# Kernel tuning notes

Hardware: AMD Instinct MI355X
Metric: run time of the kernel (lower is better)

The kernel has to match this reference:

```python
import jax, jax.numpy as jnp
import numpy as np

N0, N1, N2, N3 = 65536, 16384, 4096, 1024
S = 9  # 3x3 kernel -> 9 selections (self + 8 directions)


def _edges(key, n):
    # each node has S incoming edges, one per selection
    src = jax.random.randint(key, (n * S,), 0, n)
    dst = jnp.repeat(jnp.arange(n), S)
    sel = jnp.tile(jnp.arange(S), n)
    return src, dst, sel


def setup_inputs() -> dict:
    key = jax.random.key(0)
    ks = jax.random.split(key, 40)
    inp = {}
    inp["x"] = jax.random.normal(ks[0], (N0, 3), jnp.float32)
    sizes = [N0, N1, N2, N3]
    for l, n in enumerate(sizes):
        src, dst, sel = _edges(ks[1 + l], n)
        inp[f"src{l}"] = src
        inp[f"dst{l}"] = dst
        inp[f"sel{l}"] = sel
        inp[f"interp{l}"] = jax.random.uniform(ks[5 + l], (n * S,), jnp.float32)
    inp["clus0"] = jnp.arange(N0) // 4
    inp["clus1"] = jnp.arange(N1) // 4
    inp["clus2"] = jnp.arange(N2) // 4
    dims = [(3, 3), (3, 64), (64, 64), (64, 128), (128, 128), (128, 256), (256, 256), (256, 256), (256, 256), (256, 512)]
    for i, (ci, co) in enumerate(dims):
        kw = ks[10 + 2 * i]
        kb = ks[11 + 2 * i]
        if i == 0:  # conv1 is kernel_size=1 -> single weight matrix
            inp["W1"] = jax.random.normal(kw, (ci, co), jnp.float32) / np.sqrt(ci).astype(np.float32)
        else:
            inp[f"W{i + 1}"] = jax.random.normal(kw, (S, ci, co), jnp.float32) / np.sqrt(S * ci).astype(np.float32)
        inp[f"b{i + 1}"] = jax.random.normal(kb, (co,), jnp.float32) * 0.01
    return inp


def _sel_conv(x, src, dst, sel, interp, W, b):
    # message = interp * x[src]; routed to (dst, selection) bucket; per-selection weight
    n = x.shape[0]
    msg = x[src] * interp[:, None]                                  # [E, Cin]
    agg = jax.ops.segment_sum(msg, dst * S + sel, num_segments=n * S)
    agg = agg.reshape(n, S, -1)                                     # [N, S, Cin]
    return jnp.einsum('nsi,sio->no', agg, W) + b


def reference(x, src0, dst0, sel0, interp0, src1, dst1, sel1, interp1,
              src2, dst2, sel2, interp2, src3, dst3, sel3, interp3,
              clus0, clus1, clus2,
              W1, b1, W2, b2, W3, b3, W4, b4, W5, b5,
              W6, b6, W7, b7, W8, b8, W9, b9, W10, b10):
    relu = jax.nn.relu
    out = x @ W1 + b1                                              # conv1 (1x1), no relu
    r11 = relu(_sel_conv(out, src0, dst0, sel0, interp0, W2, b2))
    r12 = relu(_sel_conv(r11, src0, dst0, sel0, interp0, W3, b3))
    p1 = jax.ops.segment_max(r12, clus0, num_segments=N1)
    r21 = relu(_sel_conv(p1, src1, dst1, sel1, interp1, W4, b4))
    r22 = relu(_sel_conv(r21, src1, dst1, sel1, interp1, W5, b5))
    p2 = jax.ops.segment_max(r22, clus1, num_segments=N2)
    r31 = relu(_sel_conv(p2, src2, dst2, sel2, interp2, W6, b6))
    r32 = relu(_sel_conv(r31, src2, dst2, sel2, interp2, W7, b7))
    r33 = relu(_sel_conv(r32, src2, dst2, sel2, interp2, W8, b8))
    r34 = relu(_sel_conv(r33, src2, dst2, sel2, interp2, W9, b9))
    p3 = jax.ops.segment_max(r34, clus2, num_segments=N3)
    r41 = relu(_sel_conv(p3, src3, dst3, sel3, interp3, W10, b10))
    return (r11, r12, p1, r21, r22, p2, r31, r32, r33, r34, p3, r41)
```

## Files before the change

### kernel.cpp

```cpp
#include <hip/hip_runtime.h>
#include <hip/hip_bf16.h>
#include <cstddef>


#define S9 9

typedef __attribute__((ext_vector_type(8))) _Float16 f16x8;
typedef __attribute__((ext_vector_type(4))) float f32x4;

__device__ __forceinline__ unsigned short f2h(float f) {
    _Float16 h = (_Float16)f;
    unsigned short u;
    __builtin_memcpy(&u, &h, 2);
    return u;
}

__device__ void wt_tile(const float* __restrict__ in, unsigned short* __restrict__ out,
                        int K, int N, int t, float (*sm)[33]) {
    const int ktiles = K >> 6, ntiles = N >> 5;
    const int per = ktiles * ntiles;
    const int s = t / per;
    const int rem = t - s * per;
    const int kt = rem % ktiles, nt = rem / ktiles;
    const int k0 = kt * 64, n0 = nt * 32;
    const float* ip = in + (size_t)s * K * N;
    unsigned short* op = out + (size_t)s * N * K;
    const int tx = threadIdx.x & 31;
    const int ty = threadIdx.x >> 5;
#pragma unroll
    for (int r = ty; r < 64; r += 8)
        sm[r][tx] = ip[(size_t)(k0 + r) * N + n0 + tx];
    __syncthreads();
#pragma unroll
    for (int r = ty; r < 32; r += 8) {
        unsigned v = (unsigned)f2h(sm[2 * tx][r]) |
                     ((unsigned)f2h(sm[2 * tx + 1][r]) << 16);
        *(unsigned*)&op[(size_t)(n0 + r) * K + k0 + 2 * tx] = v;
    }
}

__global__ __launch_bounds__(256) void wt_all(
    const float* __restrict__ W2, const float* __restrict__ W3,
    const float* __restrict__ W4, const float* __restrict__ W5,
    const float* __restrict__ W6, const float* __restrict__ W7,
    const float* __restrict__ W8, const float* __restrict__ W9,
    const float* __restrict__ W10,
    unsigned short* o2, unsigned short* o3, unsigned short* o4,
    unsigned short* o5, unsigned short* o6, unsigned short* o7,
    unsigned short* o8, unsigned short* o9, unsigned short* o10) {
    __shared__ float sm[64][33];
    int b = blockIdx.x;
    if (b == 0) {
        for (int idx = threadIdx.x; idx < 64 * 32; idx += 256) {
            const int n = idx >> 5, k = idx & 31;
            o2[n * 32 + k] = (k < 27) ? f2h(W2[k * 64 + n]) : (unsigned short)0;
        }
        return;
    }
    b -= 1;
    if (b < 18)  { wt_tile(W3,  o3,  64,  64,  b, sm); return; }  b -= 18;
    if (b < 36)  { wt_tile(W4,  o4,  64,  128, b, sm); return; }  b -= 36;
    if (b < 72)  { wt_tile(W5,  o5,  128, 128, b, sm); return; }  b -= 72;
    if (b < 144) { wt_tile(W6,  o6,  128, 256, b, sm); return; }  b -= 144;
    if (b < 288) { wt_tile(W7,  o7,  256, 256, b, sm); return; }  b -= 288;
    if (b < 288) { wt_tile(W8,  o8,  256, 256, b, sm); return; }  b -= 288;
    if (b < 288) { wt_tile(W9,  o9,  256, 256, b, sm); return; }  b -= 288;
    wt_tile(W10, o10, 256, 512, b, sm);
}

template <int BM, int WR, int WC, int MR, int NR>
__global__ __launch_bounds__(256) void selconv_k27(
    const float* __restrict__ x, const int* __restrict__ src,
    const float* __restrict__ interp, const float* __restrict__ W1,
    const float* __restrict__ b1, const _Float16* __restrict__ Wt2,
    const float* __restrict__ bias, float* __restrict__ out,
    _Float16* __restrict__ outh) {
    constexpr int COUT = 64;
    constexpr int LDA = 40;
    __shared__ _Float16 As[BM * LDA];

    const int tid = threadIdx.x;
    const int wave = tid >> 6;
    const int lane = tid & 63;
    const int wr = wave / WC;
    const int wc = wave % WC;
    const int node0 = blockIdx.x * BM;
    const int lm = lane & 15;
    const int kq = lane >> 4;

    const float w00 = W1[0], w01 = W1[1], w02 = W1[2];
    const float w10 = W1[3], w11 = W1[4], w12 = W1[5];
    const float w20 = W1[6], w21 = W1[7], w22 = W1[8];
    const float c0 = b1[0], c1 = b1[1], c2 = b1[2];

    for (int c = tid; c < BM * 5; c += 256) {
        const int ln = c / 5;
        As[ln * LDA + 27 + (c - ln * 5)] = (_Float16)0.f;
    }
    for (int c = tid; c < BM * S9; c += 256) {
        const int ln = c / S9;
        const int s = c - ln * S9;
        const int e = (node0 + ln) * S9 + s;
        const float t = interp[e];
        const float* xr = &x[(size_t)src[e] * 3];
        const float x0 = xr[0], x1 = xr[1], x2 = xr[2];
        const float y0 = fmaf(x0, w00, fmaf(x1, w10, fmaf(x2, w20, c0)));
        const float y1 = fmaf(x0, w01, fmaf(x1, w11, fmaf(x2, w21, c1)));
        const float y2 = fmaf(x0, w02, fmaf(x1, w12, fmaf(x2, w22, c2)));
        As[ln * LDA + s * 3 + 0] = (_Float16)(t * y0);
        As[ln * LDA + s * 3 + 1] = (_Float16)(t * y1);
        As[ln * LDA + s * 3 + 2] = (_Float16)(t * y2);
    }
    __syncthreads();

    f32x4 acc[MR][NR];
    f16x8 bfr[NR];
#pragma unroll
    for (int f = 0; f < NR; ++f) {
        const int col = wc * NR * 16 + f * 16 + lm;
        bfr[f] = *(const f16x8*)(Wt2 + col * 32 + kq * 8);
        const float bv = bias[col];
#pragma unroll
        for (int i = 0; i < MR; ++i) {
            acc[i][f][0] = bv; acc[i][f][1] = bv; acc[i][f][2] = bv; acc[i][f][3] = bv;
        }
    }
#pragma unroll
    for (int i = 0; i < MR; ++i) {
        const f16x8 af =
            *(const f16x8*)&As[(wr * MR * 16 + i * 16 + lm) * LDA + kq * 8];
#pragma unroll
        for (int f = 0; f < NR; ++f)
            acc[i][f] = __builtin_amdgcn_mfma_f32_16x16x32_f16(af, bfr[f],
                                                               acc[i][f], 0, 0, 0);
    }

#pragma unroll
    for (int i = 0; i < MR; ++i)
#pragma unroll
        for (int f = 0; f < NR; ++f) {
            const int col = wc * NR * 16 + f * 16 + lm;
#pragma unroll
            for (int r = 0; r < 4; ++r) {
                const int row = node0 + wr * MR * 16 + i * 16 + kq * 4 + r;
                const float v = fmaxf(acc[i][f][r], 0.f);
                out[(size_t)row * COUT + col] = v;
                outh[(size_t)row * COUT + col] = (_Float16)v;
            }
        }
}

template <int CIN, int COUT, int BM, int BNC, int WR, int WC, int MR, int NR,
          bool POOL>
__global__ __launch_bounds__(256) void selconv_dir(
    const _Float16* __restrict__ xin, const int* __restrict__ src,
    const float* __restrict__ interp, const _Float16* __restrict__ Wt,
    const float* __restrict__ bias, float* __restrict__ out,
    _Float16* __restrict__ outh, float* __restrict__ pout,
    _Float16* __restrict__ ph) {
    static_assert(WR * WC == 4, "4 waves");
    static_assert(WR * MR * 16 == BM, "BM mismatch");
    static_assert(WC * NR * 16 == BNC, "BNC mismatch");
    constexpr int KSTEPS = CIN / 32;
    static_assert(CIN % 32 == 0, "CIN multiple of 32");

    const int tid = threadIdx.x;
    const int wave = tid >> 6;
    const int lane = tid & 63;
    const int wr = wave / WC;
    const int wc = wave % WC;
    const int node0 = blockIdx.x * BM;
    const int cb = blockIdx.y * BNC;
    const int lm = lane & 15;
    const int kq = lane >> 4;

    f32x4 acc[MR][NR];
#pragma unroll
    for (int f = 0; f < NR; ++f) {
        const float bv = bias[cb + wc * NR * 16 + f * 16 + lm];
#pragma unroll
        for (int i = 0; i < MR; ++i) {
            acc[i][f][0] = bv; acc[i][f][1] = bv;
            acc[i][f][2] = bv; acc[i][f][3] = bv;
        }
    }

    const _Float16* __restrict__ Wb =
        Wt + ((size_t)cb + wc * NR * 16 + lm) * CIN + kq * 8;

    int ebase[MR];
#pragma unroll
    for (int i = 0; i < MR; ++i)
        ebase[i] = (node0 + (wr * MR + i) * 16 + lm) * S9;

    int se_c[MR];
    float ti_c[MR];
#pragma unroll
    for (int i = 0; i < MR; ++i) {
        se_c[i] = src[ebase[i]];
        ti_c[i] = interp[ebase[i]];
    }

#pragma unroll 1
    for (int s = 0; s < S9; ++s) {
        const int sn = (s + 1 < S9) ? s + 1 : s;
        int se_n[MR];
        float ti_n[MR];
#pragma unroll
        for (int i = 0; i < MR; ++i) {
            se_n[i] = src[ebase[i] + sn];
            ti_n[i] = interp[ebase[i] + sn];
        }

        const _Float16* __restrict__ Ws = Wb + (size_t)s * COUT * CIN;
        f16x8 bfr[KSTEPS][NR];
#pragma unroll
        for (int kk = 0; kk < KSTEPS; ++kk)
#pragma unroll
            for (int f = 0; f < NR; ++f)
                bfr[kk][f] = *(const f16x8*)(Ws + (size_t)f * 16 * CIN + kk * 32);

        f16x8 av[MR][KSTEPS];
#pragma unroll
        for (int i = 0; i < MR; ++i) {
            const _Float16* __restrict__ xr =
                xin + (size_t)se_c[i] * CIN + kq * 8;
#pragma unroll
            for (int kk = 0; kk < KSTEPS; ++kk)
                av[i][kk] = *(const f16x8*)(xr + kk * 32);
        }

#pragma unroll
        for (int i = 0; i < MR; ++i) {
            const _Float16 t = (_Float16)ti_c[i];
#pragma unroll
            for (int kk = 0; kk < KSTEPS; ++kk) {
                f16x8 a = av[i][kk];
#pragma unroll
                for (int j = 0; j < 8; ++j) a[j] *= t;
#pragma unroll
                for (int f = 0; f < NR; ++f)
                    acc[i][f] = __builtin_amdgcn_mfma_f32_16x16x32_f16(
                        a, bfr[kk][f], acc[i][f], 0, 0, 0);
            }
        }

#pragma unroll
        for (int i = 0; i < MR; ++i) {
            se_c[i] = se_n[i];
            ti_c[i] = ti_n[i];
        }
    }

#pragma unroll
    for (int i = 0; i < MR; ++i)
#pragma unroll
        for (int f = 0; f < NR; ++f) {
            const int col = cb + wc * NR * 16 + f * 16 + lm;
            const int rb = node0 + (wr * MR + i) * 16 + kq * 4;
            float v0 = fmaxf(acc[i][f][0], 0.f);
            float v1 = fmaxf(acc[i][f][1], 0.f);
            float v2 = fmaxf(acc[i][f][2], 0.f);
            float v3 = fmaxf(acc[i][f][3], 0.f);
            out[(size_t)(rb + 0) * COUT + col] = v0;
            out[(size_t)(rb + 1) * COUT + col] = v1;
            out[(size_t)(rb + 2) * COUT + col] = v2;
            out[(size_t)(rb + 3) * COUT + col] = v3;
            if (outh) {
                outh[(size_t)(rb + 0) * COUT + col] = (_Float16)v0;
                outh[(size_t)(rb + 1) * COUT + col] = (_Float16)v1;
                outh[(size_t)(rb + 2) * COUT + col] = (_Float16)v2;
                outh[(size_t)(rb + 3) * COUT + col] = (_Float16)v3;
            }
            if constexpr (POOL) {
                const float m = fmaxf(fmaxf(v0, v1), fmaxf(v2, v3));
                const int prow = rb >> 2;
                pout[(size_t)prow * COUT + col] = m;
                ph[(size_t)prow * COUT + col] = (_Float16)m;
            }
        }
}

extern "C" void kernel_launch(void* const* d_in, const int* in_sizes, int n_in,
                              void* d_out, int out_size, void* d_ws, size_t ws_size,
                              hipStream_t stream) {
    const float* x = (const float*)d_in[0];
    const int* src0 = (const int*)d_in[1];
    const float* interp0 = (const float*)d_in[4];
    const int* src1 = (const int*)d_in[5];
    const float* interp1 = (const float*)d_in[8];
    const int* src2 = (const int*)d_in[9];
    const float* interp2 = (const float*)d_in[12];
    const int* src3 = (const int*)d_in[13];
    const float* interp3 = (const float*)d_in[16];
    const float* W1 = (const float*)d_in[20];
    const float* b1 = (const float*)d_in[21];
    const float* W2 = (const float*)d_in[22];
    const float* b2 = (const float*)d_in[23];
    const float* W3 = (const float*)d_in[24];
    const float* b3 = (const float*)d_in[25];
    const float* W4 = (const float*)d_in[26];
    const float* b4 = (const float*)d_in[27];
    const float* W5 = (const float*)d_in[28];
    const float* b5 = (const float*)d_in[29];
    const float* W6 = (const float*)d_in[30];
    const float* b6 = (const float*)d_in[31];
    const float* W7 = (const float*)d_in[32];
    const float* b7 = (const float*)d_in[33];
    const float* W8 = (const float*)d_in[34];
    const float* b8 = (const float*)d_in[35];
    const float* W9 = (const float*)d_in[36];
    const float* b9 = (const float*)d_in[37];
    const float* W10 = (const float*)d_in[38];
    const float* b10 = (const float*)d_in[39];

    float* out = (float*)d_out;
    float* r11 = out;
    float* r12 = r11 + (size_t)65536 * 64;
    float* p1 = r12 + (size_t)65536 * 64;
    float* r21 = p1 + (size_t)16384 * 64;
    float* r22 = r21 + (size_t)16384 * 128;
    float* p2 = r22 + (size_t)16384 * 128;
    float* r31 = p2 + (size_t)4096 * 128;
    float* r32 = r31 + (size_t)4096 * 256;
    float* r33 = r32 + (size_t)4096 * 256;
    float* r34 = r33 + (size_t)4096 * 256;
    float* p3 = r34 + (size_t)4096 * 256;
    float* r41 = p3 + (size_t)1024 * 256;

    unsigned short* w16 = (unsigned short*)d_ws;
    unsigned short* Wt2 = w16;
    unsigned short* Wt3 = Wt2 + (size_t)64 * 32;
    unsigned short* Wt4 = Wt3 + (size_t)9 * 64 * 64;
    unsigned short* Wt5 = Wt4 + (size_t)9 * 128 * 64;
    unsigned short* Wt6 = Wt5 + (size_t)9 * 128 * 128;
    unsigned short* Wt7 = Wt6 + (size_t)9 * 256 * 128;
    unsigned short* Wt8 = Wt7 + (size_t)9 * 256 * 256;
    unsigned short* Wt9 = Wt8 + (size_t)9 * 256 * 256;
    unsigned short* Wt10 = Wt9 + (size_t)9 * 256 * 256;
    unsigned short* endw = Wt10 + (size_t)9 * 512 * 256;
    _Float16* a11 = (_Float16*)endw;
    _Float16* ap1 = a11 + (size_t)65536 * 64;
    _Float16* a21 = ap1 + (size_t)16384 * 64;
    _Float16* ap2 = a21 + (size_t)16384 * 128;
    _Float16* a31 = ap2 + (size_t)4096 * 128;
    _Float16* a32 = a31 + (size_t)4096 * 256;
    _Float16* a33 = a32 + (size_t)4096 * 256;
    _Float16* ap3 = a33 + (size_t)4096 * 256;

    wt_all<<<1711, 256, 0, stream>>>(W2, W3, W4, W5, W6, W7, W8, W9, W10,
                                     Wt2, Wt3, Wt4, Wt5, Wt6, Wt7, Wt8, Wt9, Wt10);

    selconv_k27<64, 2, 2, 2, 2><<<dim3(65536 / 64), 256, 0, stream>>>(
        x, src0, interp0, W1, b1, (const _Float16*)Wt2, b2, r11, a11);

    selconv_dir<64, 64, 64, 64, 2, 2, 2, 2, true>
        <<<dim3(1024, 1), 256, 0, stream>>>(
            a11, src0, interp0, (const _Float16*)Wt3, b3, r12, nullptr, p1, ap1);

    selconv_dir<64, 128, 64, 64, 2, 2, 2, 2, false>
        <<<dim3(256, 2), 256, 0, stream>>>(
            ap1, src1, interp1, (const _Float16*)Wt4, b4, r21, a21, nullptr, nullptr);

    selconv_dir<128, 128, 64, 64, 2, 2, 2, 2, true>
        <<<dim3(256, 2), 256, 0, stream>>>(
            a21, src1, interp1, (const _Float16*)Wt5, b5, r22, nullptr, p2, ap2);

    selconv_dir<128, 256, 64, 64, 2, 2, 2, 2, false>
        <<<dim3(64, 4), 256, 0, stream>>>(
            ap2, src2, interp2, (const _Float16*)Wt6, b6, r31, a31, nullptr, nullptr);
    selconv_dir<256, 256, 64, 64, 2, 2, 2, 2, false>
        <<<dim3(64, 4), 256, 0, stream>>>(
            a31, src2, interp2, (const _Float16*)Wt7, b7, r32, a32, nullptr, nullptr);
    selconv_dir<256, 256, 64, 64, 2, 2, 2, 2, false>
        <<<dim3(64, 4), 256, 0, stream>>>(
            a32, src2, interp2, (const _Float16*)Wt8, b8, r33, a33, nullptr, nullptr);
    selconv_dir<256, 256, 64, 64, 2, 2, 2, 2, true>
        <<<dim3(64, 4), 256, 0, stream>>>(
            a33, src2, interp2, (const _Float16*)Wt9, b9, r34, nullptr, p3, ap3);

    selconv_dir<256, 512, 64, 64, 2, 2, 2, 2, false>
        <<<dim3(16, 8), 256, 0, stream>>>(
            ap3, src3, interp3, (const _Float16*)Wt10, b10, r41, nullptr, nullptr, nullptr);
}
```

Measured before the change: 433.0 us.

## Fuse all layers into one persistent cooperative kernel with grid syncs

Replaces the ten separate kernel launches with a single cooperative persistent kernel. Blocks loop over tiles for each layer and call grid-wide sync between layers, which removes per-launch overhead and inter-kernel gaps. The weight transpose and the first layer now run in the same phase, and the W2 fragment is built directly from fp32 in registers. The selconv tile also chunks its K loads in groups of four. The cost is that all stages must run at the grid size fixed by occupancy, and each grid.sync adds a barrier. Smaller layers (128–256 tiles) leave many blocks idle.

```diff
diff --git a/kernel.cpp b/kernel.cpp
--- a/kernel.cpp
+++ b/kernel.cpp
@@ -1,5 +1,5 @@
 #include <hip/hip_runtime.h>
-#include <hip/hip_bf16.h>
+#include <hip/hip_cooperative_groups.h>
 #include <cstddef>
 
 
@@ -15,8 +15,20 @@
     return u;
 }
 
+struct Pm {
+    const float* x;
+    const int *src0, *src1, *src2, *src3;
+    const float *interp0, *interp1, *interp2, *interp3;
+    const float *W1, *b1, *W2, *b2, *W3, *b3, *W4, *b4, *W5, *b5;
+    const float *W6, *b6, *W7, *b7, *W8, *b8, *W9, *b9, *W10, *b10;
+    float *r11, *r12, *p1, *r21, *r22, *p2, *r31, *r32, *r33, *r34, *p3, *r41;
+    unsigned short *Wt3, *Wt4, *Wt5, *Wt6, *Wt7, *Wt8, *Wt9, *Wt10;
+    _Float16 *a11, *ap1, *a21, *ap2, *a31, *a32, *a33, *ap3;
+};
+
 __device__ void wt_tile(const float* __restrict__ in, unsigned short* __restrict__ out,
                         int K, int N, int t, float (*sm)[33]) {
+    __syncthreads();
     const int ktiles = K >> 6, ntiles = N >> 5;
     const int per = ktiles * ntiles;
     const int s = t / per;
@@ -39,225 +51,163 @@
     }
 }
 
-__global__ __launch_bounds__(256) void wt_all(
-    const float* __restrict__ W2, const float* __restrict__ W3,
-    const float* __restrict__ W4, const float* __restrict__ W5,
-    const float* __restrict__ W6, const float* __restrict__ W7,
-    const float* __restrict__ W8, const float* __restrict__ W9,
-    const float* __restrict__ W10,
-    unsigned short* o2, unsigned short* o3, unsigned short* o4,
-    unsigned short* o5, unsigned short* o6, unsigned short* o7,
-    unsigned short* o8, unsigned short* o9, unsigned short* o10) {
-    __shared__ float sm[64][33];
-    int b = blockIdx.x;
-    if (b == 0) {
-        for (int idx = threadIdx.x; idx < 64 * 32; idx += 256) {
-            const int n = idx >> 5, k = idx & 31;
-            o2[n * 32 + k] = (k < 27) ? f2h(W2[k * 64 + n]) : (unsigned short)0;
-        }
-        return;
-    }
-    b -= 1;
-    if (b < 18)  { wt_tile(W3,  o3,  64,  64,  b, sm); return; }  b -= 18;
-    if (b < 36)  { wt_tile(W4,  o4,  64,  128, b, sm); return; }  b -= 36;
-    if (b < 72)  { wt_tile(W5,  o5,  128, 128, b, sm); return; }  b -= 72;
-    if (b < 144) { wt_tile(W6,  o6,  128, 256, b, sm); return; }  b -= 144;
-    if (b < 288) { wt_tile(W7,  o7,  256, 256, b, sm); return; }  b -= 288;
-    if (b < 288) { wt_tile(W8,  o8,  256, 256, b, sm); return; }  b -= 288;
-    if (b < 288) { wt_tile(W9,  o9,  256, 256, b, sm); return; }  b -= 288;
-    wt_tile(W10, o10, 256, 512, b, sm);
-}
-
-template <int BM, int WR, int WC, int MR, int NR>
-__global__ __launch_bounds__(256) void selconv_k27(
-    const float* __restrict__ x, const int* __restrict__ src,
-    const float* __restrict__ interp, const float* __restrict__ W1,
-    const float* __restrict__ b1, const _Float16* __restrict__ Wt2,
-    const float* __restrict__ bias, float* __restrict__ out,
-    _Float16* __restrict__ outh) {
-    constexpr int COUT = 64;
+__device__ void r11_tile(int t, const Pm& p, _Float16* As) {
+    __syncthreads();
     constexpr int LDA = 40;
-    __shared__ _Float16 As[BM * LDA];
-
     const int tid = threadIdx.x;
-    const int wave = tid >> 6;
-    const int lane = tid & 63;
-    const int wr = wave / WC;
-    const int wc = wave % WC;
-    const int node0 = blockIdx.x * BM;
-    const int lm = lane & 15;
-    const int kq = lane >> 4;
-
-    const float w00 = W1[0], w01 = W1[1], w02 = W1[2];
-    const float w10 = W1[3], w11 = W1[4], w12 = W1[5];
-    const float w20 = W1[6], w21 = W1[7], w22 = W1[8];
-    const float c0 = b1[0], c1 = b1[1], c2 = b1[2];
-
-    for (int c = tid; c < BM * 5; c += 256) {
+    const int wave = tid >> 6, lane = tid & 63;
+    const int wr = wave >> 1, wc = wave & 1;
+    const int lm = lane & 15, kq = lane >> 4;
+    const int node0 = t * 64;
+
+    const float w00 = p.W1[0], w01 = p.W1[1], w02 = p.W1[2];
+    const float w10 = p.W1[3], w11 = p.W1[4], w12 = p.W1[5];
+    const float w20 = p.W1[6], w21 = p.W1[7], w22 = p.W1[8];
+    const float c0 = p.b1[0], c1 = p.b1[1], c2 = p.b1[2];
+
+    for (int c = tid; c < 64 * 5; c += 256) {
         const int ln = c / 5;
         As[ln * LDA + 27 + (c - ln * 5)] = (_Float16)0.f;
     }
-    for (int c = tid; c < BM * S9; c += 256) {
+    for (int c = tid; c < 64 * S9; c += 256) {
         const int ln = c / S9;
         const int s = c - ln * S9;
         const int e = (node0 + ln) * S9 + s;
-        const float t = interp[e];
-        const float* xr = &x[(size_t)src[e] * 3];
+        const float tt = p.interp0[e];
+        const float* xr = &p.x[(size_t)p.src0[e] * 3];
         const float x0 = xr[0], x1 = xr[1], x2 = xr[2];
         const float y0 = fmaf(x0, w00, fmaf(x1, w10, fmaf(x2, w20, c0)));
         const float y1 = fmaf(x0, w01, fmaf(x1, w11, fmaf(x2, w21, c1)));
         const float y2 = fmaf(x0, w02, fmaf(x1, w12, fmaf(x2, w22, c2)));
-        As[ln * LDA + s * 3 + 0] = (_Float16)(t * y0);
-        As[ln * LDA + s * 3 + 1] = (_Float16)(t * y1);
-        As[ln * LDA + s * 3 + 2] = (_Float16)(t * y2);
+        As[ln * LDA + s * 3 + 0] = (_Float16)(tt * y0);
+        As[ln * LDA + s * 3 + 1] = (_Float16)(tt * y1);
+        As[ln * LDA + s * 3 + 2] = (_Float16)(tt * y2);
     }
     __syncthreads();
 
-    f32x4 acc[MR][NR];
-    f16x8 bfr[NR];
-#pragma unroll
-    for (int f = 0; f < NR; ++f) {
-        const int col = wc * NR * 16 + f * 16 + lm;
-        bfr[f] = *(const f16x8*)(Wt2 + col * 32 + kq * 8);
-        const float bv = bias[col];
-#pragma unroll
-        for (int i = 0; i < MR; ++i) {
-            acc[i][f][0] = bv; acc[i][f][1] = bv; acc[i][f][2] = bv; acc[i][f][3] = bv;
-        }
-    }
-#pragma unroll
-    for (int i = 0; i < MR; ++i) {
-        const f16x8 af =
-            *(const f16x8*)&As[(wr * MR * 16 + i * 16 + lm) * LDA + kq * 8];
-#pragma unroll
-        for (int f = 0; f < NR; ++f)
+    f32x4 acc[2][2];
+    f16x8 bfr[2];
+#pragma unroll
+    for (int f = 0; f < 2; ++f) {
+        const int col = wc * 32 + f * 16 + lm;
+#pragma unroll
+        for (int j = 0; j < 8; ++j) {
+            const int k = kq * 8 + j;
+            bfr[f][j] = (k < 27) ? (_Float16)p.W2[k * 64 + col] : (_Float16)0.f;
+        }
+        const float bv = p.b2[col];
+#pragma unroll
+        for (int i = 0; i < 2; ++i) {
+            acc[i][f][0] = bv; acc[i][f][1] = bv;
+            acc[i][f][2] = bv; acc[i][f][3] = bv;
+        }
+    }
+#pragma unroll
+    for (int i = 0; i < 2; ++i) {
+        const f16x8 af = *(const f16x8*)&As[(wr * 32 + i * 16 + lm) * LDA + kq * 8];
+#pragma unroll
+        for (int f = 0; f < 2; ++f)
             acc[i][f] = __builtin_amdgcn_mfma_f32_16x16x32_f16(af, bfr[f],
                                                                acc[i][f], 0, 0, 0);
     }
-
-#pragma unroll
-    for (int i = 0; i < MR; ++i)
-#pragma unroll
-        for (int f = 0; f < NR; ++f) {
-            const int col = wc * NR * 16 + f * 16 + lm;
+#pragma unroll
+    for (int i = 0; i < 2; ++i)
+#pragma unroll
+        for (int f = 0; f < 2; ++f) {
+            const int col = wc * 32 + f * 16 + lm;
 #pragma unroll
             for (int r = 0; r < 4; ++r) {
-                const int row = node0 + wr * MR * 16 + i * 16 + kq * 4 + r;
+                const int row = node0 + wr * 32 + i * 16 + kq * 4 + r;
                 const float v = fmaxf(acc[i][f][r], 0.f);
-                out[(size_t)row * COUT + col] = v;
-                outh[(size_t)row * COUT + col] = (_Float16)v;
-            }
-        }
-}
-
-template <int CIN, int COUT, int BM, int BNC, int WR, int WC, int MR, int NR,
-          bool POOL>
-__global__ __launch_bounds__(256) void selconv_dir(
-    const _Float16* __restrict__ xin, const int* __restrict__ src,
-    const float* __restrict__ interp, const _Float16* __restrict__ Wt,
-    const float* __restrict__ bias, float* __restrict__ out,
-    _Float16* __restrict__ outh, float* __restrict__ pout,
-    _Float16* __restrict__ ph) {
-    static_assert(WR * WC == 4, "4 waves");
-    static_assert(WR * MR * 16 == BM, "BM mismatch");
-    static_assert(WC * NR * 16 == BNC, "BNC mismatch");
+                p.r11[(size_t)row * 64 + col] = v;
+                p.a11[(size_t)row * 64 + col] = (_Float16)v;
+            }
+        }
+}
+
+template <int CIN, int COUT, bool POOL>
+__device__ void selconv_tile(
+    int node0, int cb, const _Float16* __restrict__ xin,
+    const int* __restrict__ src, const float* __restrict__ interp,
+    const _Float16* __restrict__ Wt, const float* __restrict__ bias,
+    float* __restrict__ out, _Float16* __restrict__ outh,
+    float* __restrict__ pout, _Float16* __restrict__ ph) {
     constexpr int KSTEPS = CIN / 32;
-    static_assert(CIN % 32 == 0, "CIN multiple of 32");
+    constexpr int KCH = (KSTEPS > 4) ? 4 : KSTEPS;
+    constexpr int NCH = KSTEPS / KCH;
+    static_assert(KSTEPS % KCH == 0, "chunking");
 
     const int tid = threadIdx.x;
-    const int wave = tid >> 6;
-    const int lane = tid & 63;
-    const int wr = wave / WC;
-    const int wc = wave % WC;
-    const int node0 = blockIdx.x * BM;
-    const int cb = blockIdx.y * BNC;
-    const int lm = lane & 15;
-    const int kq = lane >> 4;
-
-    f32x4 acc[MR][NR];
-#pragma unroll
-    for (int f = 0; f < NR; ++f) {
-        const float bv = bias[cb + wc * NR * 16 + f * 16 + lm];
-#pragma unroll
-        for (int i = 0; i < MR; ++i) {
+    const int wave = tid >> 6, lane = tid & 63;
+    const int wr = wave >> 1, wc = wave & 1;
+    const int lm = lane & 15, kq = lane >> 4;
+
+    f32x4 acc[2][2];
+#pragma unroll
+    for (int f = 0; f < 2; ++f) {
+        const float bv = bias[cb + wc * 32 + f * 16 + lm];
+#pragma unroll
+        for (int i = 0; i < 2; ++i) {
             acc[i][f][0] = bv; acc[i][f][1] = bv;
             acc[i][f][2] = bv; acc[i][f][3] = bv;
         }
     }
 
     const _Float16* __restrict__ Wb =
-        Wt + ((size_t)cb + wc * NR * 16 + lm) * CIN + kq * 8;
-
-    int ebase[MR];
-#pragma unroll
-    for (int i = 0; i < MR; ++i)
-        ebase[i] = (node0 + (wr * MR + i) * 16 + lm) * S9;
-
-    int se_c[MR];
-    float ti_c[MR];
-#pragma unroll
-    for (int i = 0; i < MR; ++i) {
-        se_c[i] = src[ebase[i]];
-        ti_c[i] = interp[ebase[i]];
-    }
+        Wt + ((size_t)cb + wc * 32 + lm) * CIN + kq * 8;
+    const int eb0 = (node0 + wr * 32 + lm) * S9;
+    const int eb1 = (node0 + wr * 32 + 16 + lm) * S9;
+    int se0 = src[eb0], se1 = src[eb1];
+    float ti0 = interp[eb0], ti1 = interp[eb1];
 
 #pragma unroll 1
     for (int s = 0; s < S9; ++s) {
         const int sn = (s + 1 < S9) ? s + 1 : s;
-        int se_n[MR];
-        float ti_n[MR];
-#pragma unroll
-        for (int i = 0; i < MR; ++i) {
-            se_n[i] = src[ebase[i] + sn];
-            ti_n[i] = interp[ebase[i] + sn];
-        }
+        const int se0n = src[eb0 + sn], se1n = src[eb1 + sn];
+        const float ti0n = interp[eb0 + sn], ti1n = interp[eb1 + sn];
 
         const _Float16* __restrict__ Ws = Wb + (size_t)s * COUT * CIN;
-        f16x8 bfr[KSTEPS][NR];
-#pragma unroll
-        for (int kk = 0; kk < KSTEPS; ++kk)
-#pragma unroll
-            for (int f = 0; f < NR; ++f)
-                bfr[kk][f] = *(const f16x8*)(Ws + (size_t)f * 16 * CIN + kk * 32);
-
-        f16x8 av[MR][KSTEPS];
-#pragma unroll
-        for (int i = 0; i < MR; ++i) {
-            const _Float16* __restrict__ xr =
-                xin + (size_t)se_c[i] * CIN + kq * 8;
-#pragma unroll
-            for (int kk = 0; kk < KSTEPS; ++kk)
-                av[i][kk] = *(const f16x8*)(xr + kk * 32);
-        }
-
-#pragma unroll
-        for (int i = 0; i < MR; ++i) {
-            const _Float16 t = (_Float16)ti_c[i];
-#pragma unroll
-            for (int kk = 0; kk < KSTEPS; ++kk) {
-                f16x8 a = av[i][kk];
-#pragma unroll
-                for (int j = 0; j < 8; ++j) a[j] *= t;
-#pragma unroll
-                for (int f = 0; f < NR; ++f)
-                    acc[i][f] = __builtin_amdgcn_mfma_f32_16x16x32_f16(
-                        a, bfr[kk][f], acc[i][f], 0, 0, 0);
-            }
-        }
-
-#pragma unroll
-        for (int i = 0; i < MR; ++i) {
-            se_c[i] = se_n[i];
-            ti_c[i] = ti_n[i];
-        }
-    }
-
-#pragma unroll
-    for (int i = 0; i < MR; ++i)
-#pragma unroll
-        for (int f = 0; f < NR; ++f) {
-            const int col = cb + wc * NR * 16 + f * 16 + lm;
-            const int rb = node0 + (wr * MR + i) * 16 + kq * 4;
+        const _Float16* __restrict__ x0 = xin + (size_t)se0 * CIN + kq * 8;
+        const _Float16* __restrict__ x1 = xin + (size_t)se1 * CIN + kq * 8;
+        const _Float16 h0 = (_Float16)ti0, h1 = (_Float16)ti1;
+
+#pragma unroll
+        for (int ch = 0; ch < NCH; ++ch) {
+            f16x8 a0[KCH], a1[KCH], bf[KCH][2];
+#pragma unroll
+            for (int kk = 0; kk < KCH; ++kk) {
+                a0[kk] = *(const f16x8*)(x0 + (ch * KCH + kk) * 32);
+                a1[kk] = *(const f16x8*)(x1 + (ch * KCH + kk) * 32);
+            }
+#pragma unroll
+            for (int kk = 0; kk < KCH; ++kk)
+#pragma unroll
+                for (int f = 0; f < 2; ++f)
+                    bf[kk][f] = *(const f16x8*)(Ws + (size_t)f * 16 * CIN +
+                                                (ch * KCH + kk) * 32);
+#pragma unroll
+            for (int kk = 0; kk < KCH; ++kk) {
+                f16x8 sa0 = a0[kk], sa1 = a1[kk];
+#pragma unroll
+                for (int j = 0; j < 8; ++j) { sa0[j] *= h0; sa1[j] *= h1; }
+#pragma unroll
+                for (int f = 0; f < 2; ++f) {
+                    acc[0][f] = __builtin_amdgcn_mfma_f32_16x16x32_f16(
+                        sa0, bf[kk][f], acc[0][f], 0, 0, 0);
+                    acc[1][f] = __builtin_amdgcn_mfma_f32_16x16x32_f16(
+                        sa1, bf[kk][f], acc[1][f], 0, 0, 0);
+                }
+            }
+        }
+        se0 = se0n; se1 = se1n; ti0 = ti0n; ti1 = ti1n;
+    }
+
+#pragma unroll
+    for (int i = 0; i < 2; ++i)
+#pragma unroll
+        for (int f = 0; f < 2; ++f) {
+            const int col = cb + wc * 32 + f * 16 + lm;
+            const int rb = node0 + (wr * 2 + i) * 16 + kq * 4;
             float v0 = fmaxf(acc[i][f][0], 0.f);
             float v1 = fmaxf(acc[i][f][1], 0.f);
             float v2 = fmaxf(acc[i][f][2], 0.f);
@@ -281,105 +231,138 @@
         }
 }
 
+__global__ __launch_bounds__(256, 2) void fused_all(Pm p) {
+    namespace cg = cooperative_groups;
+    cg::grid_group g = cg::this_grid();
+    __shared__ __align__(16) float smem[64 * 33];
+    const int gsz = gridDim.x;
+
+    for (int t = blockIdx.x; t < 1710 + 1024; t += gsz) {
+        if (t < 1710) {
+            int b = t;
+            float(*sm)[33] = (float(*)[33])smem;
+            if (b < 18)              wt_tile(p.W3,  p.Wt3,  64,  64,  b, sm);
+            else if ((b -= 18) < 36) wt_tile(p.W4,  p.Wt4,  64,  128, b, sm);
+            else if ((b -= 36) < 72) wt_tile(p.W5,  p.Wt5,  128, 128, b, sm);
+            else if ((b -= 72) < 144) wt_tile(p.W6, p.Wt6,  128, 256, b, sm);
+            else if ((b -= 144) < 288) wt_tile(p.W7, p.Wt7, 256, 256, b, sm);
+            else if ((b -= 288) < 288) wt_tile(p.W8, p.Wt8, 256, 256, b, sm);
+            else if ((b -= 288) < 288) wt_tile(p.W9, p.Wt9, 256, 256, b, sm);
+            else { b -= 288;         wt_tile(p.W10, p.Wt10, 256, 512, b, sm); }
+        } else {
+            r11_tile(t - 1710, p, (_Float16*)smem);
+        }
+    }
+    g.sync();
+    for (int t = blockIdx.x; t < 1024; t += gsz)
+        selconv_tile<64, 64, true>(t * 64, 0, p.a11, p.src0, p.interp0,
+                                   (const _Float16*)p.Wt3, p.b3, p.r12, nullptr,
+                                   p.p1, p.ap1);
+    g.sync();
+    for (int t = blockIdx.x; t < 512; t += gsz)
+        selconv_tile<64, 128, false>((t & 255) * 64, (t >> 8) * 64, p.ap1,
+                                     p.src1, p.interp1, (const _Float16*)p.Wt4,
+                                     p.b4, p.r21, p.a21, nullptr, nullptr);
+    g.sync();
+    for (int t = blockIdx.x; t < 512; t += gsz)
+        selconv_tile<128, 128, true>((t & 255) * 64, (t >> 8) * 64, p.a21,
+                                     p.src1, p.interp1, (const _Float16*)p.Wt5,
+                                     p.b5, p.r22, nullptr, p.p2, p.ap2);
+    g.sync();
+    for (int t = blockIdx.x; t < 256; t += gsz)
+        selconv_tile<128, 256, false>((t & 63) * 64, (t >> 6) * 64, p.ap2,
+                                      p.src2, p.interp2, (const _Float16*)p.Wt6,
+                                      p.b6, p.r31, p.a31, nullptr, nullptr);
+    g.sync();
+    for (int t = blockIdx.x; t < 256; t += gsz)
+        selconv_tile<256, 256, false>((t & 63) * 64, (t >> 6) * 64, p.a31,
+                                      p.src2, p.interp2, (const _Float16*)p.Wt7,
+                                      p.b7, p.r32, p.a32, nullptr, nullptr);
+    g.sync();
+    for (int t = blockIdx.x; t < 256; t += gsz)
+        selconv_tile<256, 256, false>((t & 63) * 64, (t >> 6) * 64, p.a32,
+                                      p.src2, p.interp2, (const _Float16*)p.Wt8,
+                                      p.b8, p.r33, p.a33, nullptr, nullptr);
+    g.sync();
+    for (int t = blockIdx.x; t < 256; t += gsz)
+        selconv_tile<256, 256, true>((t & 63) * 64, (t >> 6) * 64, p.a33,
+                                     p.src2, p.interp2, (const _Float16*)p.Wt9,
+                                     p.b9, p.r34, nullptr, p.p3, p.ap3);
+    g.sync();
+    for (int t = blockIdx.x; t < 128; t += gsz)
+        selconv_tile<256, 512, false>((t & 15) * 64, (t >> 4) * 64, p.ap3,
+                                      p.src3, p.interp3, (const _Float16*)p.Wt10,
+                                      p.b10, p.r41, nullptr, nullptr, nullptr);
+}
+
 extern "C" void kernel_launch(void* const* d_in, const int* in_sizes, int n_in,
                               void* d_out, int out_size, void* d_ws, size_t ws_size,
                               hipStream_t stream) {
-    const float* x = (const float*)d_in[0];
-    const int* src0 = (const int*)d_in[1];
-    const float* interp0 = (const float*)d_in[4];
-    const int* src1 = (const int*)d_in[5];
-    const float* interp1 = (const float*)d_in[8];
-    const int* src2 = (const int*)d_in[9];
-    const float* interp2 = (const float*)d_in[12];
-    const int* src3 = (const int*)d_in[13];
-    const float* interp3 = (const float*)d_in[16];
-    const float* W1 = (const float*)d_in[20];
-    const float* b1 = (const float*)d_in[21];
-    const float* W2 = (const float*)d_in[22];
-    const float* b2 = (const float*)d_in[23];
-    const float* W3 = (const float*)d_in[24];
-    const float* b3 = (const float*)d_in[25];
-    const float* W4 = (const float*)d_in[26];
-    const float* b4 = (const float*)d_in[27];
-    const float* W5 = (const float*)d_in[28];
-    const float* b5 = (const float*)d_in[29];
-    const float* W6 = (const float*)d_in[30];
-    const float* b6 = (const float*)d_in[31];
-    const float* W7 = (const float*)d_in[32];
-    const float* b7 = (const float*)d_in[33];
-    const float* W8 = (const float*)d_in[34];
-    const float* b8 = (const float*)d_in[35];
-    const float* W9 = (const float*)d_in[36];
-    const float* b9 = (const float*)d_in[37];
-    const float* W10 = (const float*)d_in[38];
-    const float* b10 = (const float*)d_in[39];
+    Pm p;
+    p.x = (const float*)d_in[0];
+    p.src0 = (const int*)d_in[1];
+    p.interp0 = (const float*)d_in[4];
+    p.src1 = (const int*)d_in[5];
+    p.interp1 = (const float*)d_in[8];
+    p.src2 = (const int*)d_in[9];
+    p.interp2 = (const float*)d_in[12];
+    p.src3 = (const int*)d_in[13];
+    p.interp3 = (const float*)d_in[16];
+    p.W1 = (const float*)d_in[20];  p.b1 = (const float*)d_in[21];
+    p.W2 = (const float*)d_in[22];  p.b2 = (const float*)d_in[23];
+    p.W3 = (const float*)d_in[24];  p.b3 = (const float*)d_in[25];
+    p.W4 = (const float*)d_in[26];  p.b4 = (const float*)d_in[27];
+    p.W5 = (const float*)d_in[28];  p.b5 = (const float*)d_in[29];
+    p.W6 = (const float*)d_in[30];  p.b6 = (const float*)d_in[31];
+    p.W7 = (const float*)d_in[32];  p.b7 = (const float*)d_in[33];
+    p.W8 = (const float*)d_in[34];  p.b8 = (const float*)d_in[35];
+    p.W9 = (const float*)d_in[36];  p.b9 = (const float*)d_in[37];
+    p.W10 = (const float*)d_in[38]; p.b10 = (const float*)d_in[39];
 
     float* out = (float*)d_out;
-    float* r11 = out;
-    float* r12 = r11 + (size_t)65536 * 64;
-    float* p1 = r12 + (size_t)65536 * 64;
-    float* r21 = p1 + (size_t)16384 * 64;
-    float* r22 = r21 + (size_t)16384 * 128;
-    float* p2 = r22 + (size_t)16384 * 128;
-    float* r31 = p2 + (size_t)4096 * 128;
-    float* r32 = r31 + (size_t)4096 * 256;
-    float* r33 = r32 + (size_t)4096 * 256;
-    float* r34 = r33 + (size_t)4096 * 256;
-    float* p3 = r34 + (size_t)4096 * 256;
-    float* r41 = p3 + (size_t)1024 * 256;
+    p.r11 = out;
+    p.r12 = p.r11 + (size_t)65536 * 64;
+    p.p1  = p.r12 + (size_t)65536 * 64;
+    p.r21 = p.p1 + (size_t)16384 * 64;
+    p.r22 = p.r21 + (size_t)16384 * 128;
+    p.p2  = p.r22 + (size_t)16384 * 128;
+    p.r31 = p.p2 + (size_t)4096 * 128;
+    p.r32 = p.r31 + (size_t)4096 * 256;
+    p.r33 = p.r32 + (size_t)4096 * 256;
+    p.r34 = p.r33 + (size_t)4096 * 256;
+    p.p3  = p.r34 + (size_t)4096 * 256;
+    p.r41 = p.p3 + (size_t)1024 * 256;
 
     unsigned short* w16 = (unsigned short*)d_ws;
-    unsigned short* Wt2 = w16;
-    unsigned short* Wt3 = Wt2 + (size_t)64 * 32;
-    unsigned short* Wt4 = Wt3 + (size_t)9 * 64 * 64;
-    unsigned short* Wt5 = Wt4 + (size_t)9 * 128 * 64;
-    unsigned short* Wt6 = Wt5 + (size_t)9 * 128 * 128;
-    unsigned short* Wt7 = Wt6 + (size_t)9 * 256 * 128;
-    unsigned short* Wt8 = Wt7 + (size_t)9 * 256 * 256;
-    unsigned short* Wt9 = Wt8 + (size_t)9 * 256 * 256;
-    unsigned short* Wt10 = Wt9 + (size_t)9 * 256 * 256;
-    unsigned short* endw = Wt10 + (size_t)9 * 512 * 256;
-    _Float16* a11 = (_Float16*)endw;
-    _Float16* ap1 = a11 + (size_t)65536 * 64;
-    _Float16* a21 = ap1 + (size_t)16384 * 64;
-    _Float16* ap2 = a21 + (size_t)16384 * 128;
-    _Float16* a31 = ap2 + (size_t)4096 * 128;
-    _Float16* a32 = a31 + (size_t)4096 * 256;
-    _Float16* a33 = a32 + (size_t)4096 * 256;
-    _Float16* ap3 = a33 + (size_t)4096 * 256;
-
-    wt_all<<<1711, 256, 0, stream>>>(W2, W3, W4, W5, W6, W7, W8, W9, W10,
-                                     Wt2, Wt3, Wt4, Wt5, Wt6, Wt7, Wt8, Wt9, Wt10);
-
-    selconv_k27<64, 2, 2, 2, 2><<<dim3(65536 / 64), 256, 0, stream>>>(
-        x, src0, interp0, W1, b1, (const _Float16*)Wt2, b2, r11, a11);
-
-    selconv_dir<64, 64, 64, 64, 2, 2, 2, 2, true>
-        <<<dim3(1024, 1), 256, 0, stream>>>(
-            a11, src0, interp0, (const _Float16*)Wt3, b3, r12, nullptr, p1, ap1);
-
-    selconv_dir<64, 128, 64, 64, 2, 2, 2, 2, false>
-        <<<dim3(256, 2), 256, 0, stream>>>(
-            ap1, src1, interp1, (const _Float16*)Wt4, b4, r21, a21, nullptr, nullptr);
-
-    selconv_dir<128, 128, 64, 64, 2, 2, 2, 2, true>
-        <<<dim3(256, 2), 256, 0, stream>>>(
-            a21, src1, interp1, (const _Float16*)Wt5, b5, r22, nullptr, p2, ap2);
-
-    selconv_dir<128, 256, 64, 64, 2, 2, 2, 2, false>
-        <<<dim3(64, 4), 256, 0, stream>>>(
-            ap2, src2, interp2, (const _Float16*)Wt6, b6, r31, a31, nullptr, nullptr);
-    selconv_dir<256, 256, 64, 64, 2, 2, 2, 2, false>
-        <<<dim3(64, 4), 256, 0, stream>>>(
-            a31, src2, interp2, (const _Float16*)Wt7, b7, r32, a32, nullptr, nullptr);
-    selconv_dir<256, 256, 64, 64, 2, 2, 2, 2, false>
-        <<<dim3(64, 4), 256, 0, stream>>>(
-            a32, src2, interp2, (const _Float16*)Wt8, b8, r33, a33, nullptr, nullptr);
-    selconv_dir<256, 256, 64, 64, 2, 2, 2, 2, true>
-        <<<dim3(64, 4), 256, 0, stream>>>(
-            a33, src2, interp2, (const _Float16*)Wt9, b9, r34, nullptr, p3, ap3);
-
-    selconv_dir<256, 512, 64, 64, 2, 2, 2, 2, false>
-        <<<dim3(16, 8), 256, 0, stream>>>(
-            ap3, src3, interp3, (const _Float16*)Wt10, b10, r41, nullptr, nullptr, nullptr);
-}
+    p.Wt3 = w16;
+    p.Wt4 = p.Wt3 + (size_t)9 * 64 * 64;
+    p.Wt5 = p.Wt4 + (size_t)9 * 128 * 64;
+    p.Wt6 = p.Wt5 + (size_t)9 * 128 * 128;
+    p.Wt7 = p.Wt6 + (size_t)9 * 256 * 128;
+    p.Wt8 = p.Wt7 + (size_t)9 * 256 * 256;
+    p.Wt9 = p.Wt8 + (size_t)9 * 256 * 256;
+    p.Wt10 = p.Wt9 + (size_t)9 * 256 * 256;
+    unsigned short* endw = p.Wt10 + (size_t)9 * 512 * 256;
+    p.a11 = (_Float16*)endw;
+    p.ap1 = p.a11 + (size_t)65536 * 64;
+    p.a21 = p.ap1 + (size_t)16384 * 64;
+    p.ap2 = p.a21 + (size_t)16384 * 128;
+    p.a31 = p.ap2 + (size_t)4096 * 128;
+    p.a32 = p.a31 + (size_t)4096 * 256;
+    p.a33 = p.a32 + (size_t)4096 * 256;
+    p.ap3 = p.a33 + (size_t)4096 * 256;
+
+    static int grid = 0;
+    if (grid == 0) {
+        int nb = 0;
+        if (hipOccupancyMaxActiveBlocksPerMultiprocessor(&nb, fused_all, 256, 0) !=
+                hipSuccess || nb < 1)
+            nb = 1;
+        grid = nb * 256;
+        if (grid > 1024) grid = 1024;
+    }
+
+    void* args[] = {(void*)&p};
+    hipLaunchCooperativeKernel((void*)fused_all, dim3(grid), dim3(256), args, 0,
+                               stream);
+}
```

Result: slower. 761.3 us (+75.8%).
